# Optimization experiments

Measured on AMD Instinct MI355X. Metric: run time of the kernel, lower is better.

## Reference

```python
import jax, jax.numpy as jnp
import numpy as np

B, H, N, D = 4, 8, 4096, 64
F = 64  # nb_features; must equal D because the original code multiplies k_prime (..f) elementwise with v (..d)


def setup_inputs() -> dict:
    key = jax.random.key(0)
    kq, kk, kv, kp = jax.random.split(key, 4)
    # scale inputs so exp(x @ proj.T) stays in fp32 range
    q = jax.random.normal(kq, (B, H, N, D), dtype=jnp.float32) * 0.05
    k = jax.random.normal(kk, (B, H, N, D), dtype=jnp.float32) * 0.05
    v = jax.random.normal(kv, (B, H, N, D), dtype=jnp.float32)
    proj = jax.random.normal(kp, (F, D), dtype=jnp.float32)
    return {"q": q, "k": k, "v": v, "proj": proj}


def reference(q, k, v, proj):
    # exp-kernel feature map: [b,h,n,d] x [f,d] -> [b,h,n,f]
    q_prime = jnp.exp(jnp.einsum('bhnd,fd->bhnf', q, proj))
    k_prime = jnp.exp(jnp.einsum('bhnd,fd->bhnf', k, proj))
    # denominator: sum_f q_prime * (sum_n k_prime + eps) -> [b,h,n]
    k_sum = k_prime.sum(axis=2) + 1e-6                      # [b,h,f]
    d_inv = 1.0 / jnp.einsum('bhnf,bhf->bhn', q_prime, k_sum)
    # context: elementwise product summed over sequence (requires f == d)
    ctx = (k_prime * v).sum(axis=2)                         # [b,h,d]
    out = q_prime * ctx[:, :, None, :] * d_inv[..., None]   # [b,h,n,d]
    return out
```

## Files before the change

### kernel.cpp

```cpp
#include <hip/hip_runtime.h>


#define NHEADS 32
#define SEQ    4096
#define DDIM   64
#define ACC_FLOATS (NHEADS * 128)
#define LOG2E 1.44269504088896341f

typedef __attribute__((ext_vector_type(8))) short short8;
typedef __attribute__((ext_vector_type(4))) float floatx4;

__device__ __forceinline__ short f2bf(float x) {
    unsigned int u = __float_as_uint(x);
    u += 0x7fffu + ((u >> 16) & 1u);
    return (short)(u >> 16);
}

__device__ __forceinline__ short8 cvt8(floatx4 a, floatx4 b) {
    short8 t;
    t[0] = f2bf(a[0]); t[1] = f2bf(a[1]); t[2] = f2bf(a[2]); t[3] = f2bf(a[3]);
    t[4] = f2bf(b[0]); t[5] = f2bf(b[1]); t[6] = f2bf(b[2]); t[7] = f2bf(b[3]);
    return t;
}

__device__ __forceinline__ void load_bfrag_ws(const short* __restrict__ pbf,
                                              int lane, short8 bfrag[4][2]) {
#pragma unroll
    for (int ft = 0; ft < 4; ++ft)
#pragma unroll
        for (int half = 0; half < 2; ++half)
            bfrag[ft][half] = *(const short8*)(pbf + (ft * 2 + half) * 512 + lane * 8);
}

__global__ __launch_bounds__(128) void fa_prep(const float* __restrict__ proj,
                                               float* __restrict__ ws) {
    const int tid = threadIdx.x;
    if (blockIdx.x < 32) {
        ws[blockIdx.x * 128 + tid] = 0.0f;
        return;
    }
    short* pbf = (short*)(ws + ACC_FLOATS);
#pragma unroll
    for (int i = 0; i < 32; ++i) {
        int idx  = tid * 32 + i;
        int ft2h = idx >> 9;
        int rem  = idx & 511;
        int lane = rem >> 3;
        int j    = rem & 7;
        int ft   = ft2h >> 1;
        int half = ft2h & 1;
        int fp   = lane & 15;
        int g    = lane >> 4;
        pbf[idx] = f2bf(proj[(fp * 4 + ft) * DDIM + half * 32 + g * 8 + j] * LOG2E);
    }
}

__global__ __launch_bounds__(256, 4) void fa_pass1(const float* __restrict__ K,
                                                   const float* __restrict__ V,
                                                   float* __restrict__ ws) {
    const int head = blockIdx.x >> 5;
    const int seg  = blockIdx.x & 31;
    const int tid  = threadIdx.x;
    const int w    = tid >> 6;
    const int lane = tid & 63;
    const int fp   = lane & 15;
    const int g    = lane >> 4;
    const long hbase = (long)head * SEQ;
    const int rowb = seg * 128 + w * 16;

    floatx4 kraw[2][4];
#pragma unroll
    for (int it = 0; it < 2; ++it) {
        const float* ap = K + (hbase + rowb + it * 64 + fp) * DDIM;
        kraw[it][0] = *(const floatx4*)(ap + g * 8);
        kraw[it][1] = *(const floatx4*)(ap + g * 8 + 4);
        kraw[it][2] = *(const floatx4*)(ap + 32 + g * 8);
        kraw[it][3] = *(const floatx4*)(ap + 32 + g * 8 + 4);
    }
    floatx4 vraw[2][4];
#pragma unroll
    for (int it = 0; it < 2; ++it)
#pragma unroll
        for (int r = 0; r < 4; ++r)
            vraw[it][r] =
                *(const floatx4*)(V + (hbase + rowb + it * 64 + g * 4 + r) * DDIM + fp * 4);

    const short* pbf = (const short*)(ws + ACC_FLOATS);
    short8 bfrag[4][2];
    load_bfrag_ws(pbf, lane, bfrag);

    float ksum[4] = {0.f, 0.f, 0.f, 0.f};
    float ctx[4]  = {0.f, 0.f, 0.f, 0.f};

#pragma unroll
    for (int it = 0; it < 2; ++it) {
        short8 a0 = cvt8(kraw[it][0], kraw[it][1]);
        short8 a1 = cvt8(kraw[it][2], kraw[it][3]);

        floatx4 acc[4];
#pragma unroll
        for (int ft = 0; ft < 4; ++ft) {
            floatx4 z = {0.f, 0.f, 0.f, 0.f};
            z = __builtin_amdgcn_mfma_f32_16x16x32_bf16(a0, bfrag[ft][0], z, 0, 0, 0);
            z = __builtin_amdgcn_mfma_f32_16x16x32_bf16(a1, bfrag[ft][1], z, 0, 0, 0);
            acc[ft] = z;
        }
#pragma unroll
        for (int r = 0; r < 4; ++r) {
#pragma unroll
            for (int ft = 0; ft < 4; ++ft) {
                float kp = __builtin_amdgcn_exp2f(acc[ft][r]);
                ksum[ft] += kp;
                ctx[ft]  += kp * vraw[it][r][ft];
            }
        }
    }

#pragma unroll
    for (int ft = 0; ft < 4; ++ft) {
        ksum[ft] += __shfl_xor(ksum[ft], 16); ksum[ft] += __shfl_xor(ksum[ft], 32);
        ctx[ft]  += __shfl_xor(ctx[ft], 16);  ctx[ft]  += __shfl_xor(ctx[ft], 32);
    }

    __shared__ float red[4][128];
    if (lane < 16) {
#pragma unroll
        for (int ft = 0; ft < 4; ++ft) {
            red[w][fp * 4 + ft]      = ksum[ft];
            red[w][64 + fp * 4 + ft] = ctx[ft];
        }
    }
    __syncthreads();
    if (tid < 128) {
        float s = red[0][tid] + red[1][tid] + red[2][tid] + red[3][tid];
        atomicAdd(ws + head * 128 + tid, s);
    }
}

__global__ __launch_bounds__(256, 4) void fa_pass2(const float* __restrict__ Q,
                                                   const float* __restrict__ ws,
                                                   float* __restrict__ out) {
    const int head = blockIdx.x >> 6;
    const int seg  = blockIdx.x & 63;
    const int tid  = threadIdx.x;
    const int w    = tid >> 6;
    const int lane = tid & 63;
    const int fp   = lane & 15;
    const int g    = lane >> 4;
    const long hbase = (long)head * SEQ;
    const int row0 = seg * 64 + w * 16;

    const float* ap = Q + (hbase + row0 + fp) * DDIM;
    floatx4 qraw[4];
    qraw[0] = *(const floatx4*)(ap + g * 8);
    qraw[1] = *(const floatx4*)(ap + g * 8 + 4);
    qraw[2] = *(const floatx4*)(ap + 32 + g * 8);
    qraw[3] = *(const floatx4*)(ap + 32 + g * 8 + 4);

    const short* pbf = (const short*)(ws + ACC_FLOATS);
    short8 bfrag[4][2];
    load_bfrag_ws(pbf, lane, bfrag);

    floatx4 ksr  = *(const floatx4*)(ws + head * 128 + fp * 4);
    floatx4 ctxr = *(const floatx4*)(ws + head * 128 + 64 + fp * 4);
#pragma unroll
    for (int ft = 0; ft < 4; ++ft) ksr[ft] += 1e-6f;

    short8 afrag0 = cvt8(qraw[0], qraw[1]);
    short8 afrag1 = cvt8(qraw[2], qraw[3]);

    float qp[4][4];
    float denom[4] = {0.f, 0.f, 0.f, 0.f};
#pragma unroll
    for (int ft = 0; ft < 4; ++ft) {
        floatx4 z = {0.f, 0.f, 0.f, 0.f};
        z = __builtin_amdgcn_mfma_f32_16x16x32_bf16(afrag0, bfrag[ft][0], z, 0, 0, 0);
        z = __builtin_amdgcn_mfma_f32_16x16x32_bf16(afrag1, bfrag[ft][1], z, 0, 0, 0);
#pragma unroll
        for (int r = 0; r < 4; ++r) {
            float e = __builtin_amdgcn_exp2f(z[r]);
            qp[ft][r] = e;
            denom[r] += e * ksr[ft];
        }
    }

#pragma unroll
    for (int r = 0; r < 4; ++r) {
        denom[r] += __shfl_xor(denom[r], 1);
        denom[r] += __shfl_xor(denom[r], 2);
        denom[r] += __shfl_xor(denom[r], 4);
        denom[r] += __shfl_xor(denom[r], 8);
        denom[r] = 1.0f / denom[r];
    }

#pragma unroll
    for (int r = 0; r < 4; ++r) {
        floatx4 o;
#pragma unroll
        for (int ft = 0; ft < 4; ++ft)
            o[ft] = qp[ft][r] * ctxr[ft] * denom[r];
        *(floatx4*)(out + (hbase + row0 + g * 4 + r) * DDIM + fp * 4) = o;
    }
}

extern "C" void kernel_launch(void* const* d_in, const int* in_sizes, int n_in,
                              void* d_out, int out_size, void* d_ws, size_t ws_size,
                              hipStream_t stream) {
    const float* q    = (const float*)d_in[0];
    const float* k    = (const float*)d_in[1];
    const float* v    = (const float*)d_in[2];
    const float* proj = (const float*)d_in[3];
    float* out = (float*)d_out;
    float* ws  = (float*)d_ws;

    fa_prep<<<33, 128, 0, stream>>>(proj, ws);
    fa_pass1<<<NHEADS * 32, 256, 0, stream>>>(k, v, ws);
    fa_pass2<<<NHEADS * 64, 256, 0, stream>>>(q, ws, out);
}
```

Before: 137.2 us.

## Drop prep kernel, build proj table in LDS, replace atomics with partial-sum reduction

```diff
diff --git a/kernel.cpp b/kernel.cpp
--- a/kernel.cpp
+++ b/kernel.cpp
@@ -4,7 +4,6 @@
 #define NHEADS 32
 #define SEQ    4096
 #define DDIM   64
-#define ACC_FLOATS (NHEADS * 128)
 #define LOG2E 1.44269504088896341f
 
 typedef __attribute__((ext_vector_type(8))) short short8;
@@ -23,98 +22,92 @@
     return t;
 }
 
-__device__ __forceinline__ void load_bfrag_ws(const short* __restrict__ pbf,
-                                              int lane, short8 bfrag[4][2]) {
-#pragma unroll
-    for (int ft = 0; ft < 4; ++ft)
-#pragma unroll
-        for (int half = 0; half < 2; ++half)
-            bfrag[ft][half] = *(const short8*)(pbf + (ft * 2 + half) * 512 + lane * 8);
-}
-
-__global__ __launch_bounds__(128) void fa_prep(const float* __restrict__ proj,
-                                               float* __restrict__ ws) {
-    const int tid = threadIdx.x;
-    if (blockIdx.x < 32) {
-        ws[blockIdx.x * 128 + tid] = 0.0f;
-        return;
-    }
-    short* pbf = (short*)(ws + ACC_FLOATS);
-#pragma unroll
-    for (int i = 0; i < 32; ++i) {
-        int idx  = tid * 32 + i;
-        int ft2h = idx >> 9;
-        int rem  = idx & 511;
-        int lane = rem >> 3;
-        int j    = rem & 7;
-        int ft   = ft2h >> 1;
-        int half = ft2h & 1;
-        int fp   = lane & 15;
-        int g    = lane >> 4;
-        pbf[idx] = f2bf(proj[(fp * 4 + ft) * DDIM + half * 32 + g * 8 + j] * LOG2E);
+__device__ __forceinline__ void build_tbl(const float* __restrict__ proj,
+                                          int tid, short* tbl) {
+    const float* pp = proj + tid * 16;
+    floatx4 p0 = *(const floatx4*)(pp);
+    floatx4 p1 = *(const floatx4*)(pp + 4);
+    floatx4 p2 = *(const floatx4*)(pp + 8);
+    floatx4 p3 = *(const floatx4*)(pp + 12);
+    float vals[16];
+    *(floatx4*)(vals)      = p0;
+    *(floatx4*)(vals + 4)  = p1;
+    *(floatx4*)(vals + 8)  = p2;
+    *(floatx4*)(vals + 12) = p3;
+    const int f     = tid >> 2;
+    const int dbase = (tid & 3) * 16;
+    const int ft    = f & 3;
+    const int fpp   = f >> 2;
+#pragma unroll
+    for (int i = 0; i < 16; ++i) {
+        int d    = dbase + i;
+        int half = d >> 5;
+        int gg   = (d >> 3) & 3;
+        int j    = d & 7;
+        tbl[(ft * 2 + half) * 512 + (gg * 16 + fpp) * 8 + j] = f2bf(vals[i] * LOG2E);
     }
 }
 
 __global__ __launch_bounds__(256, 4) void fa_pass1(const float* __restrict__ K,
                                                    const float* __restrict__ V,
+                                                   const float* __restrict__ proj,
                                                    float* __restrict__ ws) {
-    const int head = blockIdx.x >> 5;
-    const int seg  = blockIdx.x & 31;
+    const int head = blockIdx.x >> 6;
+    const int seg  = blockIdx.x & 63;
     const int tid  = threadIdx.x;
     const int w    = tid >> 6;
     const int lane = tid & 63;
     const int fp   = lane & 15;
     const int g    = lane >> 4;
     const long hbase = (long)head * SEQ;
-    const int rowb = seg * 128 + w * 16;
-
-    floatx4 kraw[2][4];
-#pragma unroll
-    for (int it = 0; it < 2; ++it) {
-        const float* ap = K + (hbase + rowb + it * 64 + fp) * DDIM;
-        kraw[it][0] = *(const floatx4*)(ap + g * 8);
-        kraw[it][1] = *(const floatx4*)(ap + g * 8 + 4);
-        kraw[it][2] = *(const floatx4*)(ap + 32 + g * 8);
-        kraw[it][3] = *(const floatx4*)(ap + 32 + g * 8 + 4);
-    }
-    floatx4 vraw[2][4];
-#pragma unroll
-    for (int it = 0; it < 2; ++it)
-#pragma unroll
-        for (int r = 0; r < 4; ++r)
-            vraw[it][r] =
-                *(const floatx4*)(V + (hbase + rowb + it * 64 + g * 4 + r) * DDIM + fp * 4);
-
-    const short* pbf = (const short*)(ws + ACC_FLOATS);
+    const int rowb = seg * 64 + w * 16;
+
+    __shared__ __align__(16) short tbl[4096];
+    __shared__ __align__(16) float red[4][128];
+
+    const float* ap = K + (hbase + rowb + fp) * DDIM;
+    floatx4 kraw[4];
+    kraw[0] = *(const floatx4*)(ap + g * 8);
+    kraw[1] = *(const floatx4*)(ap + g * 8 + 4);
+    kraw[2] = *(const floatx4*)(ap + 32 + g * 8);
+    kraw[3] = *(const floatx4*)(ap + 32 + g * 8 + 4);
+    floatx4 vraw[4];
+#pragma unroll
+    for (int r = 0; r < 4; ++r)
+        vraw[r] = *(const floatx4*)(V + (hbase + rowb + g * 4 + r) * DDIM + fp * 4);
+
+    build_tbl(proj, tid, tbl);
+    __syncthreads();
+
     short8 bfrag[4][2];
-    load_bfrag_ws(pbf, lane, bfrag);
+#pragma unroll
+    for (int ft = 0; ft < 4; ++ft)
+#pragma unroll
+        for (int h = 0; h < 2; ++h)
+            bfrag[ft][h] = *(const short8*)(tbl + (ft * 2 + h) * 512 + lane * 8);
+
+    short8 a0 = cvt8(kraw[0], kraw[1]);
+    short8 a1 = cvt8(kraw[2], kraw[3]);
+
+    floatx4 acc[4];
+#pragma unroll
+    for (int ft = 0; ft < 4; ++ft) {
+        floatx4 z = {0.f, 0.f, 0.f, 0.f};
+        z = __builtin_amdgcn_mfma_f32_16x16x32_bf16(a0, bfrag[ft][0], z, 0, 0, 0);
+        z = __builtin_amdgcn_mfma_f32_16x16x32_bf16(a1, bfrag[ft][1], z, 0, 0, 0);
+        acc[ft] = z;
+    }
 
     float ksum[4] = {0.f, 0.f, 0.f, 0.f};
     float ctx[4]  = {0.f, 0.f, 0.f, 0.f};
-
-#pragma unroll
-    for (int it = 0; it < 2; ++it) {
-        short8 a0 = cvt8(kraw[it][0], kraw[it][1]);
-        short8 a1 = cvt8(kraw[it][2], kraw[it][3]);
-
-        floatx4 acc[4];
+#pragma unroll
+    for (int r = 0; r < 4; ++r)
 #pragma unroll
         for (int ft = 0; ft < 4; ++ft) {
-            floatx4 z = {0.f, 0.f, 0.f, 0.f};
-            z = __builtin_amdgcn_mfma_f32_16x16x32_bf16(a0, bfrag[ft][0], z, 0, 0, 0);
-            z = __builtin_amdgcn_mfma_f32_16x16x32_bf16(a1, bfrag[ft][1], z, 0, 0, 0);
-            acc[ft] = z;
+            float kp = __builtin_amdgcn_exp2f(acc[ft][r]);
+            ksum[ft] += kp;
+            ctx[ft]  += kp * vraw[r][ft];
         }
-#pragma unroll
-        for (int r = 0; r < 4; ++r) {
-#pragma unroll
-            for (int ft = 0; ft < 4; ++ft) {
-                float kp = __builtin_amdgcn_exp2f(acc[ft][r]);
-                ksum[ft] += kp;
-                ctx[ft]  += kp * vraw[it][r][ft];
-            }
-        }
-    }
 
 #pragma unroll
     for (int ft = 0; ft < 4; ++ft) {
@@ -122,7 +115,6 @@
         ctx[ft]  += __shfl_xor(ctx[ft], 16);  ctx[ft]  += __shfl_xor(ctx[ft], 32);
     }
 
-    __shared__ float red[4][128];
     if (lane < 16) {
 #pragma unroll
         for (int ft = 0; ft < 4; ++ft) {
@@ -133,11 +125,12 @@
     __syncthreads();
     if (tid < 128) {
         float s = red[0][tid] + red[1][tid] + red[2][tid] + red[3][tid];
-        atomicAdd(ws + head * 128 + tid, s);
+        ws[(long)blockIdx.x * 128 + tid] = s;
     }
 }
 
 __global__ __launch_bounds__(256, 4) void fa_pass2(const float* __restrict__ Q,
+                                                   const float* __restrict__ proj,
                                                    const float* __restrict__ ws,
                                                    float* __restrict__ out) {
     const int head = blockIdx.x >> 6;
@@ -148,23 +141,46 @@
     const int fp   = lane & 15;
     const int g    = lane >> 4;
     const long hbase = (long)head * SEQ;
-    const int row0 = seg * 64 + w * 16;
-
-    const float* ap = Q + (hbase + row0 + fp) * DDIM;
+    const int rowb = seg * 64 + w * 16;
+
+    __shared__ __align__(16) short tbl[4096];
+    __shared__ __align__(16) float sred[2][128];
+
+    const float* ap = Q + (hbase + rowb + fp) * DDIM;
     floatx4 qraw[4];
     qraw[0] = *(const floatx4*)(ap + g * 8);
     qraw[1] = *(const floatx4*)(ap + g * 8 + 4);
     qraw[2] = *(const floatx4*)(ap + 32 + g * 8);
     qraw[3] = *(const floatx4*)(ap + 32 + g * 8 + 4);
 
-    const short* pbf = (const short*)(ws + ACC_FLOATS);
+    const int e  = tid & 127;
+    const int ph = tid >> 7;
+    const float* wp = ws + (long)head * 8192 + (long)ph * 4096 + e;
+    float s = 0.f;
+#pragma unroll
+    for (int p = 0; p < 32; ++p) s += wp[p * 128];
+
+    build_tbl(proj, tid, tbl);
+    sred[ph][e] = s;
+    __syncthreads();
+
     short8 bfrag[4][2];
-    load_bfrag_ws(pbf, lane, bfrag);
-
-    floatx4 ksr  = *(const floatx4*)(ws + head * 128 + fp * 4);
-    floatx4 ctxr = *(const floatx4*)(ws + head * 128 + 64 + fp * 4);
-#pragma unroll
-    for (int ft = 0; ft < 4; ++ft) ksr[ft] += 1e-6f;
+#pragma unroll
+    for (int ft = 0; ft < 4; ++ft)
+#pragma unroll
+        for (int h = 0; h < 2; ++h)
+            bfrag[ft][h] = *(const short8*)(tbl + (ft * 2 + h) * 512 + lane * 8);
+
+    floatx4 k0 = *(const floatx4*)(&sred[0][fp * 4]);
+    floatx4 k1 = *(const floatx4*)(&sred[1][fp * 4]);
+    floatx4 c0 = *(const floatx4*)(&sred[0][64 + fp * 4]);
+    floatx4 c1 = *(const floatx4*)(&sred[1][64 + fp * 4]);
+    floatx4 ksr, ctxr;
+#pragma unroll
+    for (int ft = 0; ft < 4; ++ft) {
+        ksr[ft]  = k0[ft] + k1[ft] + 1e-6f;
+        ctxr[ft] = c0[ft] + c1[ft];
+    }
 
     short8 afrag0 = cvt8(qraw[0], qraw[1]);
     short8 afrag1 = cvt8(qraw[2], qraw[3]);
@@ -178,9 +194,9 @@
         z = __builtin_amdgcn_mfma_f32_16x16x32_bf16(afrag1, bfrag[ft][1], z, 0, 0, 0);
 #pragma unroll
         for (int r = 0; r < 4; ++r) {
-            float e = __builtin_amdgcn_exp2f(z[r]);
-            qp[ft][r] = e;
-            denom[r] += e * ksr[ft];
+            float qe = __builtin_amdgcn_exp2f(z[r]);
+            qp[ft][r] = qe;
+            denom[r] += qe * ksr[ft];
         }
     }
 
@@ -199,7 +215,7 @@
 #pragma unroll
         for (int ft = 0; ft < 4; ++ft)
             o[ft] = qp[ft][r] * ctxr[ft] * denom[r];
-        *(floatx4*)(out + (hbase + row0 + g * 4 + r) * DDIM + fp * 4) = o;
+        *(floatx4*)(out + (hbase + rowb + g * 4 + r) * DDIM + fp * 4) = o;
     }
 }
 
@@ -213,7 +229,6 @@
     float* out = (float*)d_out;
     float* ws  = (float*)d_ws;
 
-    fa_prep<<<33, 128, 0, stream>>>(proj, ws);
-    fa_pass1<<<NHEADS * 32, 256, 0, stream>>>(k, v, ws);
-    fa_pass2<<<NHEADS * 64, 256, 0, stream>>>(q, ws, out);
-}
+    fa_pass1<<<NHEADS * 64, 256, 0, stream>>>(k, v, proj, ws);
+    fa_pass2<<<NHEADS * 64, 256, 0, stream>>>(q, proj, ws, out);
+}
```

Result: no change. 136.4 us (-0.6%).
